# Optimization experiments

Hardware: AMD Instinct MI355X
Metric: run time of the kernel (lower is better)

The kernel has to match this reference:

```python
import jax, jax.numpy as jnp
import numpy as np

B, S, HID = 2, 4096, 2048
NH, NKV, HD = 32, 8, 64
GROUPS = NH // NKV
ROPE_THETA = 10000.0


def _rope_cos_sin(seq_len, dim, dtype):
    inv_freq = 1.0 / (ROPE_THETA ** (jnp.arange(0, dim, 2, dtype=jnp.float32) / dim))
    pos = jnp.arange(seq_len, dtype=jnp.float32)
    freqs = pos[:, None] * inv_freq[None, :]          # [S, D/2]
    emb = jnp.concatenate([freqs, freqs], axis=-1)    # [S, D]
    return jnp.cos(emb).astype(dtype), jnp.sin(emb).astype(dtype)


def _rotate_half(x):
    x1, x2 = jnp.split(x, 2, axis=-1)
    return jnp.concatenate([-x2, x1], axis=-1)


def _apply_rope(x, cos, sin):
    # x: [B, H, S, D]; cos/sin: [S, D]
    return x * cos[None, None] + _rotate_half(x) * sin[None, None]


def kappa(x):
    return jax.nn.elu(x) + 1.0


def setup_inputs() -> dict:
    key = jax.random.key(0)
    ks = jax.random.split(key, 6)
    sc = 0.02
    return {
        "hidden_states": jax.random.normal(ks[0], (B, S, HID), jnp.float32),
        "Wq": jax.random.normal(ks[1], (HID, NH * HD), jnp.float32) * sc,
        "Wk": jax.random.normal(ks[2], (HID, NKV * HD), jnp.float32) * sc,
        "Wv": jax.random.normal(ks[3], (HID, NKV * HD), jnp.float32) * sc,
        "Wphi": jax.random.normal(ks[4], (HID, HID), jnp.float32) * sc,
        "Wo": jax.random.normal(ks[5], (HID, HID), jnp.float32) * sc,
    }


def reference(hidden_states, Wq, Wk, Wv, Wphi, Wo):
    bsz, q_len, _ = hidden_states.shape

    q = (hidden_states @ Wq).reshape(bsz, q_len, NH, HD).transpose(0, 2, 1, 3)   # [B,NH,S,D]
    k = (hidden_states @ Wk).reshape(bsz, q_len, NKV, HD).transpose(0, 2, 1, 3)  # [B,NKV,S,D]
    v = (hidden_states @ Wv).reshape(bsz, q_len, NKV, HD).transpose(0, 2, 1, 3)

    cos, sin = _rope_cos_sin(q_len, HD, hidden_states.dtype)
    q = _apply_rope(q, cos, sin)
    k = _apply_rope(k, cos, sin)

    # repeat_kv for GQA: [B,NKV,S,D] -> [B,NH,S,D]
    k = jnp.repeat(k, GROUPS, axis=1)
    v = jnp.repeat(v, GROUPS, axis=1)

    Qk = kappa(q)   # [B,NH,S,D]
    Kk = kappa(k)

    Qg = Qk.mean(axis=2)                                # [B,NH,D] global query
    logits = jnp.einsum("bnd,bnsd->bns", Qg, Kk)        # [B,NH,S]
    alpha = jax.nn.softmax(logits, axis=-1) * float(q_len)

    # KV aggregation: [B,NH,D,D] state
    outer_sum = jnp.einsum("bns,bnsd,bnsf->bndf", alpha, Kk, v)
    result_attn = jnp.einsum("bnsd,bndf->bnsf", Qk, outer_sum)  # [B,NH,S,D]

    X_phi = (hidden_states @ Wphi).reshape(bsz, q_len, NH, HD).transpose(0, 2, 1, 3)
    ctx = (X_phi * result_attn).transpose(0, 2, 1, 3).reshape(bsz, q_len, HID)
    return ctx @ Wo
```

## Files before the change

### kernel.cpp

```cpp
#include <hip/hip_runtime.h>
#include <hip/hip_bf16.h>

#define B_ 2
#define S_ 4096
#define HID_ 2048
#define NH_ 32
#define NKV_ 8
#define HD_ 64
#define GROUPS_ 4
#define NCH_ 32
#define NLIN_ 5120

typedef short short8 __attribute__((ext_vector_type(8)));
typedef float floatx4 __attribute__((ext_vector_type(4)));

__device__ __forceinline__ float bf2f(unsigned short u){
  union { unsigned int i; float f; } v; v.i = ((unsigned int)u) << 16; return v.f;
}
__device__ __forceinline__ unsigned short f2bf(float f){
  union { float f; unsigned int i; } v; v.f = f;
  unsigned int i = v.i;
  unsigned int r = (i + 0x7fffu + ((i >> 16) & 1u)) >> 16;
  return (unsigned short)r;
}

__device__ __forceinline__ void async_copy16(unsigned short* lds, const unsigned short* g){
  __builtin_amdgcn_global_load_lds((const __attribute__((address_space(1))) void*)g,
                                   (__attribute__((address_space(3))) void*)lds,
                                   16, 0, 0);
}

__global__ void conv_bf16(const float* __restrict__ x, unsigned short* __restrict__ y, int n4){
  int i = blockIdx.x * 256 + threadIdx.x;
  if (i < n4){
    float4 v = ((const float4*)x)[i];
    ushort4 o;
    o.x = f2bf(v.x); o.y = f2bf(v.y); o.z = f2bf(v.z); o.w = f2bf(v.w);
    ((ushort4*)y)[i] = o;
  }
}

__global__ void transpose_all(const float* __restrict__ Wq, const float* __restrict__ Wk,
                              const float* __restrict__ Wv, const float* __restrict__ Wphi,
                              const float* __restrict__ Wo,
                              unsigned short* __restrict__ wcat, unsigned short* __restrict__ wot){
  const float* W; unsigned short* Wt; int N;
  switch (blockIdx.z){
    case 0:  W = Wq;   Wt = wcat;                              N = 2048; break;
    case 1:  W = Wk;   Wt = wcat + (size_t)2048 * HID_;        N = 512;  break;
    case 2:  W = Wv;   Wt = wcat + (size_t)2560 * HID_;        N = 512;  break;
    case 3:  W = Wphi; Wt = wcat + (size_t)3072 * HID_;        N = 2048; break;
    default: W = Wo;   Wt = wot;                               N = 2048; break;
  }
  int n0 = blockIdx.x * 32, k0 = blockIdx.y * 32;
  if (n0 >= N) return;
  __shared__ float tile[32][33];
  int tx = threadIdx.x, ty = threadIdx.y;
  #pragma unroll
  for (int j = 0; j < 4; j++)
    tile[ty + j*8][tx] = W[(size_t)(k0 + ty + j*8) * N + n0 + tx];
  __syncthreads();
  #pragma unroll
  for (int j = 0; j < 4; j++)
    Wt[(size_t)(n0 + ty + j*8) * HID_ + k0 + tx] = f2bf(tile[tx][ty + j*8]);
}

#define GTILE 16384

__global__ __launch_bounds__(512, 2) void gemm256(
    const unsigned short* __restrict__ A, const unsigned short* __restrict__ Bt,
    void* __restrict__ Cv, int M, int N, int K, int cbf16)
{
  __shared__ __align__(16) unsigned short As[2 * GTILE];
  __shared__ __align__(16) unsigned short Bs[2 * GTILE];

  const int tid = threadIdx.x;
  const int w = tid >> 6, lane = tid & 63;
  const int wr = w >> 2, wc = w & 3;
  const int l15 = lane & 15, quad = lane >> 4;

  const int nbx = N >> 8;
  int flat = blockIdx.y * nbx + blockIdx.x;
  int nwg  = nbx * (M >> 8);
  int cpx  = nwg >> 3;
  int swz  = (flat & 7) * cpx + (flat >> 3);
  int bx = swz % nbx, by = swz / nbx;
  const int m0 = by << 8, n0 = bx << 8;

  const int srow = (w << 3) + (lane >> 3);
  const int scc  = (lane & 7) ^ (lane >> 3);
  const unsigned short* gA = A  + (size_t)(m0 + srow) * K + scc * 8;
  const unsigned short* gB = Bt + (size_t)(n0 + srow) * K + scc * 8;
  const size_t rs64  = (size_t)64  * K;
  const size_t rs128 = (size_t)128 * K;
  unsigned short* lA0 = As + (w << 9);
  unsigned short* lB0 = Bs + (w << 9);

#define STAGE_A(bsel, h, t) do { \
    unsigned short* _d = lA0 + (bsel) * GTILE + (h) * 8192; \
    const unsigned short* _g = gA + (size_t)(h) * rs128 + (size_t)(t) * 64; \
    async_copy16(_d, _g); \
    async_copy16(_d + 4096, _g + rs64); \
  } while (0)
#define STAGE_B(bsel, h, t) do { \
    unsigned short* _d = lB0 + (bsel) * GTILE + (h) * 8192; \
    const unsigned short* _g = gB + (size_t)(h) * rs128 + (size_t)(t) * 64; \
    async_copy16(_d, _g); \
    async_copy16(_d + 4096, _g + rs64); \
  } while (0)
#define SCHED0 __builtin_amdgcn_sched_barrier(0)

  const int ks0  = ((quad     ^ (lane & 7)) << 3);
  const int ks1  = (((4+quad) ^ (lane & 7)) << 3);
  const int arow = (wr * 128 + l15) * 64;
  const int brow = (wc * 64  + l15) * 64;

  floatx4 acc[8][4] = {};
  short8 af[8][2], bfr[4][2];

  const int nt = K >> 6;

  STAGE_A(0, 0, 0); STAGE_A(0, 1, 0); STAGE_B(0, 0, 0); STAGE_B(0, 1, 0);
  if (nt > 1){
    STAGE_A(1, 0, 1); STAGE_A(1, 1, 1); STAGE_B(1, 0, 1); STAGE_B(1, 1, 1);
    asm volatile("s_waitcnt vmcnt(8)" ::: "memory");
  } else {
    asm volatile("s_waitcnt vmcnt(0)" ::: "memory");
  }
  SCHED0;
  __builtin_amdgcn_s_barrier();
  SCHED0;

  for (int T = 0; T < nt; ++T){
    const int cb = T & 1;
    const unsigned short* Ab = As + cb * GTILE;
    const unsigned short* Bb = Bs + cb * GTILE;

    #pragma unroll
    for (int m = 0; m < 8; ++m){
      af[m][0] = *(const short8*)(Ab + arow + m * 1024 + ks0);
      af[m][1] = *(const short8*)(Ab + arow + m * 1024 + ks1);
    }
    #pragma unroll
    for (int n = 0; n < 4; ++n){
      bfr[n][0] = *(const short8*)(Bb + brow + n * 1024 + ks0);
      bfr[n][1] = *(const short8*)(Bb + brow + n * 1024 + ks1);
    }
    SCHED0; __builtin_amdgcn_s_barrier(); SCHED0;
    __builtin_amdgcn_s_setprio(1);
    #pragma unroll
    for (int k = 0; k < 2; ++k)
      #pragma unroll
      for (int m = 0; m < 4; ++m)
        #pragma unroll
        for (int n = 0; n < 4; ++n)
          acc[m][n] = __builtin_amdgcn_mfma_f32_16x16x32_bf16(af[m][k], bfr[n][k], acc[m][n], 0, 0, 0);
    __builtin_amdgcn_s_setprio(0);
    SCHED0; __builtin_amdgcn_s_barrier(); SCHED0;

    if (T + 2 < nt){
      STAGE_A(cb, 0, T + 2); STAGE_A(cb, 1, T + 2);
      STAGE_B(cb, 0, T + 2); STAGE_B(cb, 1, T + 2);
      asm volatile("s_waitcnt vmcnt(8)" ::: "memory");
    } else {
      asm volatile("s_waitcnt vmcnt(0)" ::: "memory");
    }
    SCHED0; __builtin_amdgcn_s_barrier(); SCHED0;
    __builtin_amdgcn_s_setprio(1);
    #pragma unroll
    for (int k = 0; k < 2; ++k)
      #pragma unroll
      for (int m = 0; m < 4; ++m)
        #pragma unroll
        for (int n = 0; n < 4; ++n)
          acc[4+m][n] = __builtin_amdgcn_mfma_f32_16x16x32_bf16(af[4+m][k], bfr[n][k], acc[4+m][n], 0, 0, 0);
    __builtin_amdgcn_s_setprio(0);
    SCHED0; __builtin_amdgcn_s_barrier(); SCHED0;
  }

#undef STAGE_A
#undef STAGE_B
#undef SCHED0

  if (cbf16){
    unsigned short* Cb = (unsigned short*)Cv;
    #pragma unroll
    for (int mi = 0; mi < 8; ++mi){
      const int row = m0 + wr * 128 + mi * 16 + quad * 4;
      #pragma unroll
      for (int ni = 0; ni < 4; ++ni){
        const int col = n0 + wc * 64 + ni * 16 + l15;
        #pragma unroll
        for (int r = 0; r < 4; ++r)
          Cb[(size_t)(row + r) * N + col] = f2bf(acc[mi][ni][r]);
      }
    }
  } else {
    float* Cf = (float*)Cv;
    #pragma unroll
    for (int mi = 0; mi < 8; ++mi){
      const int row = m0 + wr * 128 + mi * 16 + quad * 4;
      #pragma unroll
      for (int ni = 0; ni < 4; ++ni){
        const int col = n0 + wc * 64 + ni * 16 + l15;
        #pragma unroll
        for (int r = 0; r < 4; ++r)
          Cf[(size_t)(row + r) * N + col] = acc[mi][ni][r];
      }
    }
  }
}

__global__ void rope_fused(const unsigned short* __restrict__ lin,
                           unsigned short* __restrict__ Qk, unsigned short* __restrict__ Kk){
  int blk = blockIdx.x;
  if (blk < 32768){
    int idx = blk * 256 + threadIdx.x;
    int i = idx & 31;
    int n = (idx >> 5) & (NH_ - 1);
    int s = (idx >> 10) & (S_ - 1);
    int b = idx >> 22;
    float invf = exp2f(-(float)i * (13.287712379549449f / 32.0f));
    float ang = (float)s * invf;
    float c = cosf(ang), sn = sinf(ang);
    size_t in_o = (size_t)(b * S_ + s) * NLIN_ + n * HD_;
    float x1 = bf2f(lin[in_o + i]);
    float x2 = bf2f(lin[in_o + i + 32]);
    float r1 = x1 * c - x2 * sn;
    float r2 = x2 * c + x1 * sn;
    r1 = r1 > 0.f ? r1 + 1.f : __expf(r1);
    r2 = r2 > 0.f ? r2 + 1.f : __expf(r2);
    size_t o = ((size_t)(b * NH_ + n) * S_ + s) * HD_;
    Qk[o + i] = f2bf(r1);
    Qk[o + i + 32] = f2bf(r2);
  } else {
    int idx = (blk - 32768) * 256 + threadIdx.x;
    int i = idx & 31;
    int kv = (idx >> 5) & (NKV_ - 1);
    int s = (idx >> 8) & (S_ - 1);
    int b = idx >> 20;
    float invf = exp2f(-(float)i * (13.287712379549449f / 32.0f));
    float ang = (float)s * invf;
    float c = cosf(ang), sn = sinf(ang);
    size_t in_o = (size_t)(b * S_ + s) * NLIN_ + 2048 + kv * HD_;
    float x1 = bf2f(lin[in_o + i]);
    float x2 = bf2f(lin[in_o + i + 32]);
    float r1 = x1 * c - x2 * sn;
    float r2 = x2 * c + x1 * sn;
    r1 = r1 > 0.f ? r1 + 1.f : __expf(r1);
    r2 = r2 > 0.f ? r2 + 1.f : __expf(r2);
    size_t o = ((size_t)(b * NKV_ + kv) * S_ + s) * HD_;
    Kk[o + i] = f2bf(r1);
    Kk[o + i + 32] = f2bf(r2);
  }
}

__global__ __launch_bounds__(256) void qg_mean(const unsigned short* __restrict__ Qk,
                                               float* __restrict__ Qg){
  int bn = blockIdx.x, chunk = blockIdx.y;
  int tid = threadIdx.x;
  int dgrp = tid & 7, sgrp = tid >> 3;
  const unsigned short* base = Qk + (size_t)bn * S_ * HD_
                             + (size_t)(chunk * 256 + sgrp) * HD_ + dgrp * 8;
  float acc[8] = {};
  #pragma unroll
  for (int i = 0; i < 8; i++){
    short8 v = *(const short8*)(base + (size_t)i * 32 * HD_);
    #pragma unroll
    for (int e = 0; e < 8; e++) acc[e] += bf2f((unsigned short)v[e]);
  }
  __shared__ float red[256][8];
  #pragma unroll
  for (int e = 0; e < 8; e++) red[tid][e] = acc[e];
  __syncthreads();
  if (tid < 64){
    int dg = tid >> 3, e = tid & 7;
    float s = 0.f;
    #pragma unroll
    for (int g = 0; g < 32; g++) s += red[g * 8 + dg][e];
    atomicAdd(&Qg[bn * 64 + tid], s * (1.0f / (float)S_));
  }
}

__global__ __launch_bounds__(256) void logits_kernel(const unsigned short* __restrict__ Kk,
                                                     const float* __restrict__ Qg,
                                                     float* __restrict__ logits){
  int bn = blockIdx.x, chunk = blockIdx.y;
  int b = bn / NH_, n = bn % NH_, kv = n / GROUPS_;
  int tid = threadIdx.x;
  __shared__ float qg[64];
  if (tid < 64) qg[tid] = Qg[bn * 64 + tid];
  __syncthreads();
  int s = chunk * 256 + tid;
  const unsigned short* row = Kk + ((size_t)(b * NKV_ + kv) * S_ + s) * HD_;
  float acc = 0.f;
  #pragma unroll
  for (int c = 0; c < 8; c++){
    short8 v = *(const short8*)(row + c * 8);
    #pragma unroll
    for (int e = 0; e < 8; e++) acc += qg[c * 8 + e] * bf2f((unsigned short)v[e]);
  }
  logits[(size_t)bn * S_ + s] = acc;
}

__global__ __launch_bounds__(256) void softmax_kernel(const float* __restrict__ logits,
                                                      float* __restrict__ alpha){
  int bn = blockIdx.x;
  int tid = threadIdx.x;
  float l[16];
  float mymax = -1e30f;
  #pragma unroll
  for (int j = 0; j < 16; j++){
    l[j] = logits[(size_t)bn * S_ + j * 256 + tid];
    mymax = fmaxf(mymax, l[j]);
  }
  __shared__ float red[256];
  red[tid] = mymax; __syncthreads();
  for (int st = 128; st > 0; st >>= 1){
    if (tid < st) red[tid] = fmaxf(red[tid], red[tid + st]);
    __syncthreads();
  }
  float gmax = red[0];
  __syncthreads();
  float mysum = 0.f;
  #pragma unroll
  for (int j = 0; j < 16; j++){ l[j] = __expf(l[j] - gmax); mysum += l[j]; }
  red[tid] = mysum; __syncthreads();
  for (int st = 128; st > 0; st >>= 1){
    if (tid < st) red[tid] += red[tid + st];
    __syncthreads();
  }
  float inv = (float)S_ / red[0];
  #pragma unroll
  for (int j = 0; j < 16; j++)
    alpha[(size_t)bn * S_ + j * 256 + tid] = l[j] * inv;
}

__global__ __launch_bounds__(256) void outer_sum_kernel(const unsigned short* __restrict__ Kk,
                                                        const unsigned short* __restrict__ lin,
                                                        const float* __restrict__ alpha,
                                                        float* __restrict__ part){
  int bkv = blockIdx.x, chunk = blockIdx.y;
  int b = bkv >> 3, kv = bkv & 7;
  int tid = threadIdx.x;
  int d = tid >> 2, fb = (tid & 3) * 16;
  __shared__ float ks[64][64];
  __shared__ float vs[64][64];
  __shared__ float as4[64][4];
  float acc[4][16] = {};
  const unsigned short* kb = Kk + (size_t)(b * NKV_ + kv) * S_ * HD_;
  const int SPC = S_ / NCH_;

  for (int t = 0; t < SPC / 64; t++){
    int ss = chunk * SPC + t * 64;
    #pragma unroll
    for (int jj = 0; jj < 4; jj++){
      int idx4 = jj * 256 + tid;
      int si = idx4 >> 4, c4 = (idx4 & 15) * 4;
      ushort4 kv4 = *(const ushort4*)(kb + (size_t)(ss + si) * HD_ + c4);
      ks[si][c4]   = bf2f(kv4.x); ks[si][c4+1] = bf2f(kv4.y);
      ks[si][c4+2] = bf2f(kv4.z); ks[si][c4+3] = bf2f(kv4.w);
      ushort4 vv4 = *(const ushort4*)(lin + (size_t)(b * S_ + ss + si) * NLIN_ + 2560 + kv * HD_ + c4);
      vs[si][c4]   = bf2f(vv4.x); vs[si][c4+1] = bf2f(vv4.y);
      vs[si][c4+2] = bf2f(vv4.z); vs[si][c4+3] = bf2f(vv4.w);
    }
    {
      int si = tid >> 2, h = tid & 3;
      as4[si][h] = alpha[(size_t)(b * NH_ + kv * GROUPS_ + h) * S_ + ss + si];
    }
    __syncthreads();
    #pragma unroll 4
    for (int si = 0; si < 64; si++){
      float k = ks[si][d];
      float4 a4 = *(const float4*)&as4[si][0];
      float4 v0 = *(const float4*)&vs[si][fb];
      float4 v1 = *(const float4*)&vs[si][fb + 4];
      float4 v2 = *(const float4*)&vs[si][fb + 8];
      float4 v3 = *(const float4*)&vs[si][fb + 12];
      float ak0 = a4.x * k, ak1 = a4.y * k, ak2 = a4.z * k, ak3 = a4.w * k;
      acc[0][0]  += ak0 * v0.x; acc[0][1]  += ak0 * v0.y; acc[0][2]  += ak0 * v0.z; acc[0][3]  += ak0 * v0.w;
      acc[0][4]  += ak0 * v1.x; acc[0][5]  += ak0 * v1.y; acc[0][6]  += ak0 * v1.z; acc[0][7]  += ak0 * v1.w;
      acc[0][8]  += ak0 * v2.x; acc[0][9]  += ak0 * v2.y; acc[0][10] += ak0 * v2.z; acc[0][11] += ak0 * v2.w;
      acc[0][12] += ak0 * v3.x; acc[0][13] += ak0 * v3.y; acc[0][14] += ak0 * v3.z; acc[0][15] += ak0 * v3.w;
      acc[1][0]  += ak1 * v0.x; acc[1][1]  += ak1 * v0.y; acc[1][2]  += ak1 * v0.z; acc[1][3]  += ak1 * v0.w;
      acc[1][4]  += ak1 * v1.x; acc[1][5]  += ak1 * v1.y; acc[1][6]  += ak1 * v1.z; acc[1][7]  += ak1 * v1.w;
      acc[1][8]  += ak1 * v2.x; acc[1][9]  += ak1 * v2.y; acc[1][10] += ak1 * v2.z; acc[1][11] += ak1 * v2.w;
      acc[1][12] += ak1 * v3.x; acc[1][13] += ak1 * v3.y; acc[1][14] += ak1 * v3.z; acc[1][15] += ak1 * v3.w;
      acc[2][0]  += ak2 * v0.x; acc[2][1]  += ak2 * v0.y; acc[2][2]  += ak2 * v0.z; acc[2][3]  += ak2 * v0.w;
      acc[2][4]  += ak2 * v1.x; acc[2][5]  += ak2 * v1.y; acc[2][6]  += ak2 * v1.z; acc[2][7]  += ak2 * v1.w;
      acc[2][8]  += ak2 * v2.x; acc[2][9]  += ak2 * v2.y; acc[2][10] += ak2 * v2.z; acc[2][11] += ak2 * v2.w;
      acc[2][12] += ak2 * v3.x; acc[2][13] += ak2 * v3.y; acc[2][14] += ak2 * v3.z; acc[2][15] += ak2 * v3.w;
      acc[3][0]  += ak3 * v0.x; acc[3][1]  += ak3 * v0.y; acc[3][2]  += ak3 * v0.z; acc[3][3]  += ak3 * v0.w;
      acc[3][4]  += ak3 * v1.x; acc[3][5]  += ak3 * v1.y; acc[3][6]  += ak3 * v1.z; acc[3][7]  += ak3 * v1.w;
      acc[3][8]  += ak3 * v2.x; acc[3][9]  += ak3 * v2.y; acc[3][10] += ak3 * v2.z; acc[3][11] += ak3 * v2.w;
      acc[3][12] += ak3 * v3.x; acc[3][13] += ak3 * v3.y; acc[3][14] += ak3 * v3.z; acc[3][15] += ak3 * v3.w;
    }
    __syncthreads();
  }

  #pragma unroll
  for (int h = 0; h < 4; h++){
    float* pb = part + ((size_t)(chunk * 16 + bkv) * 4 + h) * 4096 + d * 64 + fb;
    #pragma unroll
    for (int j = 0; j < 4; j++)
      *(float4*)&pb[j * 4] = *(float4*)&acc[h][j * 4];
  }
}

__global__ __launch_bounds__(256) void osum_reduce_t(const float* __restrict__ part,
                                                     unsigned short* __restrict__ osumb){
  int bn = blockIdx.x;
  int tid = threadIdx.x;
  __shared__ float os[64][65];
  const float4* p4 = (const float4*)part;
  #pragma unroll
  for (int r = 0; r < 4; r++){
    int idx4 = r * 256 + tid;
    float4 s = {0.f, 0.f, 0.f, 0.f};
    #pragma unroll 8
    for (int c = 0; c < NCH_; c++){
      float4 v = p4[(size_t)c * 65536 + bn * 1024 + idx4];
      s.x += v.x; s.y += v.y; s.z += v.z; s.w += v.w;
    }
    int d = idx4 >> 4;
    int f0 = (idx4 & 15) * 4;
    os[d][f0] = s.x; os[d][f0+1] = s.y; os[d][f0+2] = s.z; os[d][f0+3] = s.w;
  }
  __syncthreads();
  int f = tid >> 2, d0 = (tid & 3) * 16;
  unsigned short hi[16], lo[16];
  #pragma unroll
  for (int j = 0; j < 16; j++){
    float x = os[d0 + j][f];
    unsigned short h = f2bf(x);
    hi[j] = h;
    lo[j] = f2bf(x - bf2f(h));
  }
  unsigned short* oh = osumb + ((size_t)bn * 2) * 4096 + (size_t)f * 64 + d0;
  unsigned short* ol = oh + 4096;
  *(short8*)(oh)     = *(const short8*)(hi);
  *(short8*)(oh + 8) = *(const short8*)(hi + 8);
  *(short8*)(ol)     = *(const short8*)(lo);
  *(short8*)(ol + 8) = *(const short8*)(lo + 8);
}

__global__ __launch_bounds__(256) void ctx_mfma(const unsigned short* __restrict__ Qk,
                                                const unsigned short* __restrict__ osumb,
                                                const unsigned short* __restrict__ lin,
                                                unsigned short* __restrict__ ctx){
  int bn = blockIdx.x, sc = blockIdx.y;
  int b = bn >> 5, n = bn & 31;
  int tid = threadIdx.x;
  int w = tid >> 6, lane = tid & 63;
  int l15 = lane & 15, quad = lane >> 4;

  const unsigned short* obase = osumb + ((size_t)bn * 2) * 4096;
  short8 bh[4][2], bl[4][2];
  #pragma unroll
  for (int nf = 0; nf < 4; nf++){
    int f = nf * 16 + l15;
    #pragma unroll
    for (int kh = 0; kh < 2; kh++){
      bh[nf][kh] = *(const short8*)(obase + (size_t)f * 64 + kh * 32 + quad * 8);
      bl[nf][kh] = *(const short8*)(obase + 4096 + (size_t)f * 64 + kh * 32 + quad * 8);
    }
  }

  int s0 = sc * 256 + w * 64;
  const unsigned short* qbase = Qk + ((size_t)bn * S_ + s0) * HD_;
  floatx4 acc[4][4] = {};
  #pragma unroll
  for (int m = 0; m < 4; m++){
    short8 a0 = *(const short8*)(qbase + (size_t)(m * 16 + l15) * HD_ + quad * 8);
    short8 a1 = *(const short8*)(qbase + (size_t)(m * 16 + l15) * HD_ + 32 + quad * 8);
    #pragma unroll
    for (int nf = 0; nf < 4; nf++){
      acc[m][nf] = __builtin_amdgcn_mfma_f32_16x16x32_bf16(a0, bh[nf][0], acc[m][nf], 0, 0, 0);
      acc[m][nf] = __builtin_amdgcn_mfma_f32_16x16x32_bf16(a1, bh[nf][1], acc[m][nf], 0, 0, 0);
      acc[m][nf] = __builtin_amdgcn_mfma_f32_16x16x32_bf16(a0, bl[nf][0], acc[m][nf], 0, 0, 0);
      acc[m][nf] = __builtin_amdgcn_mfma_f32_16x16x32_bf16(a1, bl[nf][1], acc[m][nf], 0, 0, 0);
    }
  }

  #pragma unroll
  for (int m = 0; m < 4; m++){
    #pragma unroll
    for (int r = 0; r < 4; r++){
      int s = s0 + m * 16 + quad * 4 + r;
      const unsigned short* xp = lin + (size_t)(b * S_ + s) * NLIN_ + 3072 + n * HD_;
      unsigned short* cp = ctx + (size_t)(b * S_ + s) * HID_ + n * HD_;
      #pragma unroll
      for (int nf = 0; nf < 4; nf++){
        int f = nf * 16 + l15;
        cp[f] = f2bf(bf2f(xp[f]) * acc[m][nf][r]);
      }
    }
  }
}

extern "C" void kernel_launch(void* const* d_in, const int* in_sizes, int n_in,
                              void* d_out, int out_size, void* d_ws, size_t ws_size,
                              hipStream_t stream) {
  const float* hs   = (const float*)d_in[0];
  const float* Wq   = (const float*)d_in[1];
  const float* Wk   = (const float*)d_in[2];
  const float* Wv   = (const float*)d_in[3];
  const float* Wphi = (const float*)d_in[4];
  const float* Wo   = (const float*)d_in[5];
  float* out = (float*)d_out;

  char* ws = (char*)d_ws;
  const size_t M = (size_t)B_ * S_;
  size_t off = 0;
  auto alloc = [&](size_t bytes){ size_t o = off; off += (bytes + 255) & ~(size_t)255; return o; };

  size_t off_x     = alloc(M * HID_ * 4);
  size_t off_wcat  = alloc((size_t)NLIN_ * HID_ * 2);
  size_t off_wot   = alloc((size_t)HID_ * HID_ * 2);
  size_t off_lin   = alloc(M * NLIN_ * 2);
  size_t off_qk    = alloc(M * HID_ * 2);
  size_t off_kk    = alloc(M * 512 * 2);
  size_t off_qg    = alloc(64 * 64 * 4);
  size_t off_alph  = alloc((size_t)B_ * NH_ * S_ * 4);
  size_t off_osumb = alloc((size_t)64 * 2 * 4096 * 2);
  (void)ws_size;

  unsigned short* hsb  = (unsigned short*)(ws + off_x);
  float*          part = (float*)(ws + off_x);
  unsigned short* ctx  = (unsigned short*)(ws + off_x);
  unsigned short* wcat = (unsigned short*)(ws + off_wcat);
  unsigned short* wot  = (unsigned short*)(ws + off_wot);
  unsigned short* lin  = (unsigned short*)(ws + off_lin);
  unsigned short* qk = (unsigned short*)(ws + off_qk);
  unsigned short* kk = (unsigned short*)(ws + off_kk);
  float* qg   = (float*)(ws + off_qg);
  float* alph = (float*)(ws + off_alph);
  unsigned short* osumb = (unsigned short*)(ws + off_osumb);

  conv_bf16<<<(int)(M * HID_ / 4 / 256), 256, 0, stream>>>(hs, hsb, (int)(M * HID_ / 4));
  transpose_all<<<dim3(64, 64, 5), dim3(32, 8), 0, stream>>>(Wq, Wk, Wv, Wphi, Wo, wcat, wot);
  gemm256<<<dim3(NLIN_/256, M/256), 512, 0, stream>>>(hsb, wcat, lin, (int)M, NLIN_, HID_, 1);
  rope_fused<<<32768 + 8192, 256, 0, stream>>>(lin, qk, kk);
  hipMemsetAsync(qg, 0, 64 * 64 * 4, stream);
  qg_mean<<<dim3(B_ * NH_, S_ / 256), 256, 0, stream>>>(qk, qg);
  logits_kernel<<<dim3(B_ * NH_, S_ / 256), 256, 0, stream>>>(kk, qg, alph);
  softmax_kernel<<<B_ * NH_, 256, 0, stream>>>(alph, alph);
  outer_sum_kernel<<<dim3(B_ * NKV_, NCH_), 256, 0, stream>>>(kk, lin, alph, part);
  osum_reduce_t<<<64, 256, 0, stream>>>(part, osumb);
  ctx_mfma<<<dim3(B_ * NH_, S_ / 64 / 4), 256, 0, stream>>>(qk, osumb, lin, ctx);
  gemm256<<<dim3(HID_/256, M/256), 512, 0, stream>>>(ctx, wot, out, (int)M, HID_, HID_, 0);
}
```

Measured before the change: 538.8 us.

## Split GEMM K-step into four quadrant phases with interleaved async staging

Reassigns each warp's output tile so it covers four 64x32-style quadrants that line up with the two staged half-tiles, instead of one contiguous 128x64 block. The K-loop now runs four MFMA phases (A0B0, A0B1, A1B0, A1B1). Between phases it loads only the LDS fragments the next phase needs and issues one half-tile async global-to-LDS copy for the next stages. This spreads global and LDS traffic across the compute and shortens the exposed load latency. In exchange there are more barriers per iteration and the vmcnt accounting and epilogue index mapping become more intricate.

```diff
diff --git a/kernel.cpp b/kernel.cpp
--- a/kernel.cpp
+++ b/kernel.cpp
@@ -112,8 +112,8 @@
 
   const int ks0  = ((quad     ^ (lane & 7)) << 3);
   const int ks1  = (((4+quad) ^ (lane & 7)) << 3);
-  const int arow = (wr * 128 + l15) * 64;
-  const int brow = (wc * 64  + l15) * 64;
+  const int arow0 = (wr * 64 + l15) * 64;
+  const int brow0 = (wc * 32 + l15) * 64;
 
   floatx4 acc[8][4] = {};
   short8 af[8][2], bfr[4][2];
@@ -122,8 +122,8 @@
 
   STAGE_A(0, 0, 0); STAGE_A(0, 1, 0); STAGE_B(0, 0, 0); STAGE_B(0, 1, 0);
   if (nt > 1){
-    STAGE_A(1, 0, 1); STAGE_A(1, 1, 1); STAGE_B(1, 0, 1); STAGE_B(1, 1, 1);
-    asm volatile("s_waitcnt vmcnt(8)" ::: "memory");
+    STAGE_A(1, 0, 1); STAGE_B(1, 0, 1); STAGE_B(1, 1, 1);
+    asm volatile("s_waitcnt vmcnt(6)" ::: "memory");
   } else {
     asm volatile("s_waitcnt vmcnt(0)" ::: "memory");
   }
@@ -137,15 +137,16 @@
     const unsigned short* Bb = Bs + cb * GTILE;
 
     #pragma unroll
-    for (int m = 0; m < 8; ++m){
-      af[m][0] = *(const short8*)(Ab + arow + m * 1024 + ks0);
-      af[m][1] = *(const short8*)(Ab + arow + m * 1024 + ks1);
-    }
-    #pragma unroll
-    for (int n = 0; n < 4; ++n){
-      bfr[n][0] = *(const short8*)(Bb + brow + n * 1024 + ks0);
-      bfr[n][1] = *(const short8*)(Bb + brow + n * 1024 + ks1);
-    }
+    for (int m = 0; m < 4; ++m){
+      af[m][0] = *(const short8*)(Ab + arow0 + m * 1024 + ks0);
+      af[m][1] = *(const short8*)(Ab + arow0 + m * 1024 + ks1);
+    }
+    #pragma unroll
+    for (int n = 0; n < 2; ++n){
+      bfr[n][0] = *(const short8*)(Bb + brow0 + n * 1024 + ks0);
+      bfr[n][1] = *(const short8*)(Bb + brow0 + n * 1024 + ks1);
+    }
+    if (T + 1 < nt){ STAGE_A(cb ^ 1, 1, T + 1); }
     SCHED0; __builtin_amdgcn_s_barrier(); SCHED0;
     __builtin_amdgcn_s_setprio(1);
     #pragma unroll
@@ -153,15 +154,50 @@
       #pragma unroll
       for (int m = 0; m < 4; ++m)
         #pragma unroll
-        for (int n = 0; n < 4; ++n)
+        for (int n = 0; n < 2; ++n)
           acc[m][n] = __builtin_amdgcn_mfma_f32_16x16x32_bf16(af[m][k], bfr[n][k], acc[m][n], 0, 0, 0);
     __builtin_amdgcn_s_setprio(0);
     SCHED0; __builtin_amdgcn_s_barrier(); SCHED0;
 
+    #pragma unroll
+    for (int n = 2; n < 4; ++n){
+      bfr[n][0] = *(const short8*)(Bb + brow0 + 8192 + (n - 2) * 1024 + ks0);
+      bfr[n][1] = *(const short8*)(Bb + brow0 + 8192 + (n - 2) * 1024 + ks1);
+    }
+    if (T + 2 < nt){ STAGE_A(cb, 0, T + 2); }
+    SCHED0; __builtin_amdgcn_s_barrier(); SCHED0;
+    __builtin_amdgcn_s_setprio(1);
+    #pragma unroll
+    for (int k = 0; k < 2; ++k)
+      #pragma unroll
+      for (int m = 0; m < 4; ++m)
+        #pragma unroll
+        for (int n = 2; n < 4; ++n)
+          acc[m][n] = __builtin_amdgcn_mfma_f32_16x16x32_bf16(af[m][k], bfr[n][k], acc[m][n], 0, 0, 0);
+    __builtin_amdgcn_s_setprio(0);
+    SCHED0; __builtin_amdgcn_s_barrier(); SCHED0;
+
+    #pragma unroll
+    for (int m = 4; m < 8; ++m){
+      af[m][0] = *(const short8*)(Ab + arow0 + 8192 + (m - 4) * 1024 + ks0);
+      af[m][1] = *(const short8*)(Ab + arow0 + 8192 + (m - 4) * 1024 + ks1);
+    }
+    if (T + 2 < nt){ STAGE_B(cb, 0, T + 2); }
+    SCHED0; __builtin_amdgcn_s_barrier(); SCHED0;
+    __builtin_amdgcn_s_setprio(1);
+    #pragma unroll
+    for (int k = 0; k < 2; ++k)
+      #pragma unroll
+      for (int m = 4; m < 8; ++m)
+        #pragma unroll
+        for (int n = 0; n < 2; ++n)
+          acc[m][n] = __builtin_amdgcn_mfma_f32_16x16x32_bf16(af[m][k], bfr[n][k], acc[m][n], 0, 0, 0);
+    __builtin_amdgcn_s_setprio(0);
+    SCHED0; __builtin_amdgcn_s_barrier(); SCHED0;
+
     if (T + 2 < nt){
-      STAGE_A(cb, 0, T + 2); STAGE_A(cb, 1, T + 2);
-      STAGE_B(cb, 0, T + 2); STAGE_B(cb, 1, T + 2);
-      asm volatile("s_waitcnt vmcnt(8)" ::: "memory");
+      STAGE_B(cb, 1, T + 2);
+      asm volatile("s_waitcnt vmcnt(6)" ::: "memory");
     } else {
       asm volatile("s_waitcnt vmcnt(0)" ::: "memory");
     }
@@ -170,10 +206,10 @@
     #pragma unroll
     for (int k = 0; k < 2; ++k)
       #pragma unroll
-      for (int m = 0; m < 4; ++m)
+      for (int m = 4; m < 8; ++m)
         #pragma unroll
-        for (int n = 0; n < 4; ++n)
-          acc[4+m][n] = __builtin_amdgcn_mfma_f32_16x16x32_bf16(af[4+m][k], bfr[n][k], acc[4+m][n], 0, 0, 0);
+        for (int n = 2; n < 4; ++n)
+          acc[m][n] = __builtin_amdgcn_mfma_f32_16x16x32_bf16(af[m][k], bfr[n][k], acc[m][n], 0, 0, 0);
     __builtin_amdgcn_s_setprio(0);
     SCHED0; __builtin_amdgcn_s_barrier(); SCHED0;
   }
@@ -186,10 +222,10 @@
     unsigned short* Cb = (unsigned short*)Cv;
     #pragma unroll
     for (int mi = 0; mi < 8; ++mi){
-      const int row = m0 + wr * 128 + mi * 16 + quad * 4;
+      const int row = m0 + (mi & 3) * 16 + wr * 64 + (mi >> 2) * 128 + quad * 4;
       #pragma unroll
       for (int ni = 0; ni < 4; ++ni){
-        const int col = n0 + wc * 64 + ni * 16 + l15;
+        const int col = n0 + (ni & 1) * 16 + wc * 32 + (ni >> 1) * 128 + l15;
         #pragma unroll
         for (int r = 0; r < 4; ++r)
           Cb[(size_t)(row + r) * N + col] = f2bf(acc[mi][ni][r]);
@@ -199,10 +235,10 @@
     float* Cf = (float*)Cv;
     #pragma unroll
     for (int mi = 0; mi < 8; ++mi){
-      const int row = m0 + wr * 128 + mi * 16 + quad * 4;
+      const int row = m0 + (mi & 3) * 16 + wr * 64 + (mi >> 2) * 128 + quad * 4;
       #pragma unroll
       for (int ni = 0; ni < 4; ++ni){
-        const int col = n0 + wc * 64 + ni * 16 + l15;
+        const int col = n0 + (ni & 1) * 16 + wc * 32 + (ni >> 1) * 128 + l15;
         #pragma unroll
         for (int r = 0; r < 4; ++r)
           Cf[(size_t)(row + r) * N + col] = acc[mi][ni][r];
```

New measurement: 516.6 us. 4.1% less time.
